# Kernel tuning notes

Hardware: AMD Instinct MI355X
Metric: run time of the kernel (lower is better)

The kernel has to match this reference:

```python
import jax, jax.numpy as jnp
import numpy as np

T = 24
ETA_C = 0.95
ETA_D = 0.95
NEG_BIG = -1e30  # finite stand-in for -inf so softmax rows stay NaN-free

# Static ragged-segment index map: for row t, entries i<t point into the flat
# X1 vector at offset t*(t-1)/2 + i (matches the Python loop's idx_nodes walk).
_t = np.arange(T)[:, None]
_i = np.arange(T)[None, :]
VALID = jnp.asarray(_i < _t)                     # (24,24) bool, strictly lower-tri
IDX = jnp.asarray(np.where(_i < _t, (_t * (_t - 1)) // 2 + _i, 0))  # (24,24) int


def make_W():
    """Fixed triangular summation weight (276,72), as built in __init__."""
    W = np.zeros((276, 72), dtype=np.float32)
    j = 0
    for t in range(1, 24):
        for i in range(t):
            W[j, i + 24] = 1.0
            W[j, i + 48] = 1.0
            W[j, i:t] += 1.0  # note i:t may overlap the i+24/i+48 cols? (it cannot: i<t<=23<24)
            j += 1
    return jnp.asarray(W)


def setup_inputs() -> dict:
    key = jax.random.key(0)
    k1, k2, k3 = jax.random.split(key, 3)
    return {
        "pi_s": jax.random.uniform(k1, (T,), dtype=jnp.float32),
        "pi_c": jax.random.uniform(k2, (T,), dtype=jnp.float32),
        "pi_g": jax.random.uniform(k3, (T,), dtype=jnp.float32),
        "B": jnp.ones((1,), dtype=jnp.float32) * 5.0,
        "W": make_W(),
    }


def reference(pi_s, pi_c, pi_g, B, W):
    # X = [pi_s/eta_d, pi_c/(eta_c*eta_d), pi_g]  -> (72,)
    X = jnp.concatenate([pi_s / ETA_D, pi_c / (ETA_C * ETA_D), pi_g])
    X1 = W @ X  # (276,) flat ragged segments

    E = X1[IDX]  # (24,24): row t holds its t candidate prices (garbage where ~VALID)
    # X2[t] = min over the t-element window; row 0 has no valid entries -> +inf
    X2 = jnp.min(jnp.where(VALID, E, jnp.inf), axis=1)
    # X3[t,:t] = softmin(B * e_t) = softmax(-B * e_t); rows 0 zeroed out
    logits = jnp.where(VALID, -B[0] * E, NEG_BIG)
    X3 = jnp.where(VALID, jax.nn.softmax(logits, axis=1), 0.0)
    return X2, X3
```

## Files before the change

kernel.cpp:

```cpp
#include <hip/hip_runtime.h>
#include <math.h>
#include <float.h>

#define TT 24
#define NSEG 276
#define XD 72

__global__ __launch_bounds__(256) void fused_segsoftmin_kernel(
    const float* __restrict__ pi_s,
    const float* __restrict__ pi_c,
    const float* __restrict__ pi_g,
    const float* __restrict__ Bp,
    const float* __restrict__ W,
    float* __restrict__ out)
{
    __shared__ float sX[XD];
    __shared__ float sX1[NSEG];

    const int tid = threadIdx.x;

    if (tid < XD) {
        const float etacd = (float)(0.95 * 0.95);
        float v;
        if (tid < 24)       v = pi_s[tid] / 0.95f;
        else if (tid < 48)  v = pi_c[tid - 24] / etacd;
        else                v = pi_g[tid - 48];
        sX[tid] = v;
    }
    __syncthreads();

    for (int j = tid; j < NSEG; j += 256) {
        const float* wr = W + j * XD;
        float acc = 0.0f;
        #pragma unroll
        for (int k = 0; k < XD; ++k) acc += wr[k] * sX[k];
        sX1[j] = acc;
    }
    __syncthreads();

    if (tid < TT) {
        const int t = tid;
        float* __restrict__ x2  = out;
        float* __restrict__ row = out + TT + t * TT;

        if (t == 0) {
            x2[0] = 1.0e30f;
            #pragma unroll
            for (int i = 0; i < TT; ++i) row[i] = 0.0f;
        } else {
            const float B = Bp[0];
            const int base = (t * (t - 1)) >> 1;

            float mn = INFINITY;
            float mx = -INFINITY;
            for (int i = 0; i < t; ++i) {
                const float e = sX1[base + i];
                mn = fminf(mn, e);
                mx = fmaxf(mx, -B * e);
            }
            x2[t] = mn;

            float denom = 0.0f;
            for (int i = 0; i < t; ++i) {
                const float p = expf(-B * sX1[base + i] - mx);
                row[i] = p;
                denom += p;
            }
            const float inv = 1.0f / denom;
            for (int i = 0; i < t; ++i) row[i] *= inv;
            for (int i = t; i < TT; ++i) row[i] = 0.0f;
        }
    }
}

extern "C" void kernel_launch(void* const* d_in, const int* in_sizes, int n_in,
                              void* d_out, int out_size, void* d_ws, size_t ws_size,
                              hipStream_t stream) {
    const float* pi_s = (const float*)d_in[0];
    const float* pi_c = (const float*)d_in[1];
    const float* pi_g = (const float*)d_in[2];
    const float* B    = (const float*)d_in[3];
    const float* W    = (const float*)d_in[4];
    float* out = (float*)d_out;

    fused_segsoftmin_kernel<<<1, 256, 0, stream>>>(pi_s, pi_c, pi_g, B, W, out);
}
```

Before: 68.67 us.

## Replace W matmul with closed-form suffix sums and shrink block to 64

Drops the dense 276x72 matrix-vector product against W and computes each segment value directly as a running suffix sum of scaled pi_s plus pi_c/eta+pi_g. The goal is to remove the global W reads and the per-row 72-term dot products. It also keeps exponentials in registers instead of a read-modify-write on output, and launches 64 threads instead of 256. The kernel now assumes W has exactly the fixed triangular structure and ignores its contents.

```diff
diff --git a/kernel.cpp b/kernel.cpp
--- a/kernel.cpp
+++ b/kernel.cpp
@@ -3,10 +3,8 @@
 #include <float.h>
 
 #define TT 24
-#define NSEG 276
-#define XD 72
 
-__global__ __launch_bounds__(256) void fused_segsoftmin_kernel(
+__global__ __launch_bounds__(64) void fused_segsoftmin_kernel(
     const float* __restrict__ pi_s,
     const float* __restrict__ pi_c,
     const float* __restrict__ pi_g,
@@ -14,32 +12,20 @@
     const float* __restrict__ W,
     float* __restrict__ out)
 {
-    __shared__ float sX[XD];
-    __shared__ float sX1[NSEG];
+    __shared__ float sPS[TT];
+    __shared__ float sPCG[TT];
 
-    const int tid = threadIdx.x;
+    const int t = threadIdx.x;
+    (void)W;
 
-    if (tid < XD) {
+    if (t < TT) {
         const float etacd = (float)(0.95 * 0.95);
-        float v;
-        if (tid < 24)       v = pi_s[tid] / 0.95f;
-        else if (tid < 48)  v = pi_c[tid - 24] / etacd;
-        else                v = pi_g[tid - 48];
-        sX[tid] = v;
+        sPS[t]  = pi_s[t] / 0.95f;
+        sPCG[t] = pi_c[t] / etacd + pi_g[t];
     }
     __syncthreads();
 
-    for (int j = tid; j < NSEG; j += 256) {
-        const float* wr = W + j * XD;
-        float acc = 0.0f;
-        #pragma unroll
-        for (int k = 0; k < XD; ++k) acc += wr[k] * sX[k];
-        sX1[j] = acc;
-    }
-    __syncthreads();
-
-    if (tid < TT) {
-        const int t = tid;
+    if (t < TT) {
         float* __restrict__ x2  = out;
         float* __restrict__ row = out + TT + t * TT;
 
@@ -49,25 +35,28 @@
             for (int i = 0; i < TT; ++i) row[i] = 0.0f;
         } else {
             const float B = Bp[0];
-            const int base = (t * (t - 1)) >> 1;
 
+            float e[TT];
+            float run = 0.0f;
             float mn = INFINITY;
             float mx = -INFINITY;
-            for (int i = 0; i < t; ++i) {
-                const float e = sX1[base + i];
-                mn = fminf(mn, e);
-                mx = fmaxf(mx, -B * e);
+            for (int i = t - 1; i >= 0; --i) {
+                run += sPS[i];
+                const float ei = sPCG[i] + run;
+                e[i] = ei;
+                mn = fminf(mn, ei);
+                mx = fmaxf(mx, -B * ei);
             }
             x2[t] = mn;
 
             float denom = 0.0f;
             for (int i = 0; i < t; ++i) {
-                const float p = expf(-B * sX1[base + i] - mx);
-                row[i] = p;
+                const float p = expf(-B * e[i] - mx);
+                e[i] = p;
                 denom += p;
             }
             const float inv = 1.0f / denom;
-            for (int i = 0; i < t; ++i) row[i] *= inv;
+            for (int i = 0; i < t; ++i) row[i] = e[i] * inv;
             for (int i = t; i < TT; ++i) row[i] = 0.0f;
         }
     }
@@ -83,5 +72,5 @@
     const float* W    = (const float*)d_in[4];
     float* out = (float*)d_out;
 
-    fused_segsoftmin_kernel<<<1, 256, 0, stream>>>(pi_s, pi_c, pi_g, B, W, out);
+    fused_segsoftmin_kernel<<<1, 64, 0, stream>>>(pi_s, pi_c, pi_g, B, W, out);
 }
```

Result: faster. 65.30 us (-4.9%).
